# Kernel optimization log

Hardware: AMD Instinct MI355X
Metric: run time of the kernel (lower is better)

## Reference

```python
import jax, jax.numpy as jnp
import numpy as np

# Complete binary Huffman tree: V leaves, V-1 internal nodes, heap-indexed
# (node 0 = root, leaf i lives at heap index V-1+i, parent(n) = (n-1)//2).
V = 32768     # vocab size (leaves)
D = 15        # path depth = log2(V) internal nodes per leaf
DM = 1024     # input word-vector dim
B = 8         # batch of input word vectors
T = 1024      # target ids per batch item


def _build_paths():
    """paths[i, l] = heap index of the l-th internal node (leaf-to-root) on leaf i's path."""
    n = np.arange(V, dtype=np.int64) + (V - 1)  # leaf heap indices
    paths = np.zeros((V, D), dtype=np.int32)
    for lvl in range(D):
        n = (n - 1) // 2
        paths[:, lvl] = n
    return jnp.asarray(paths)


def setup_inputs() -> dict:
    key = jax.random.key(0)
    k1, k2, k3 = jax.random.split(key, 3)
    x = jax.random.normal(k1, (B, DM), dtype=jnp.float32)
    ids = jax.random.randint(k2, (B, T), 0, V)
    W = jax.random.normal(k3, (V - 1, DM), dtype=jnp.float32) * 0.02  # stacked Linear(DM,1) weights
    b = jnp.zeros((V - 1,), dtype=jnp.float32)                        # stacked Linear biases
    return {"x": x, "ids": ids, "paths": _build_paths(), "W": W, "b": b}


def reference(x, ids, paths, W, b):
    # node_idx: [B, T, D] internal-node heap indices along each target's path
    node_idx = paths[ids]
    Wp = W[node_idx]                 # [B, T, D, DM] gathered per-node weight rows
    bp = b[node_idx]                 # [B, T, D]
    # per-node Linear + bias: logit = w_node . x + b_node
    logits = jnp.einsum('btdk,bk->btd', Wp, x) + bp
    # product of sigmoid branch probabilities along the path -> [B, T]
    return jnp.prod(jax.nn.sigmoid(logits), axis=-1)
```

## Files before the change

kernel.cpp:

```cpp
#include <hip/hip_runtime.h>
#include <math.h>

#define V 32768
#define D 15
#define DM 1024
#define B 8
#define T 1024
#define NNODES (V - 1)
#define R 4

__global__ __launch_bounds__(256, 4) void hsm_logits_kernel(
    const float* __restrict__ x,
    const float* __restrict__ W,
    const float* __restrict__ bias,
    float* __restrict__ sig)
{
    __shared__ float4 xs[B * DM / 4];

    const float4* x4 = (const float4*)x;
    #pragma unroll
    for (int i = threadIdx.x; i < B * DM / 4; i += 256) xs[i] = x4[i];
    __syncthreads();

    const int wave = threadIdx.x >> 6;
    const int lane = threadIdx.x & 63;
    const int row0 = (blockIdx.x * 4 + wave) * R;

    const float4* Wb = (const float4*)W;
    const float4* Wr[R];
    #pragma unroll
    for (int r = 0; r < R; r++) {
        int row = row0 + r;
        if (row > NNODES - 1) row = NNODES - 1;
        Wr[r] = Wb + (size_t)row * 256;
    }

    float acc[R * B];
    #pragma unroll
    for (int i = 0; i < R * B; i++) acc[i] = 0.f;

    #pragma unroll
    for (int j = 0; j < 4; j++) {
        const int u = j * 64 + lane;
        float4 wv[R];
        #pragma unroll
        for (int r = 0; r < R; r++) wv[r] = Wr[r][u];
        float4 xv[B];
        #pragma unroll
        for (int b = 0; b < B; b++) xv[b] = xs[b * 256 + u];
        #pragma unroll
        for (int r = 0; r < R; r++) {
            #pragma unroll
            for (int b = 0; b < B; b++) {
                acc[r * 8 + b] += wv[r].x * xv[b].x + wv[r].y * xv[b].y +
                                  wv[r].z * xv[b].z + wv[r].w * xv[b].w;
            }
        }
    }

#define FOLD_LEVEL(MASK, NOUT)                                   \
    _Pragma("unroll")                                            \
    for (int i = 0; i < (NOUT); i++) {                           \
        const float lo = acc[2 * i];                             \
        const float hi = acc[2 * i + 1];                         \
        const float send = (lane & (MASK)) ? lo : hi;            \
        const float keep = (lane & (MASK)) ? hi : lo;            \
        acc[i] = keep + __shfl_xor(send, (MASK), 64);            \
    }
    FOLD_LEVEL(1, 16)
    FOLD_LEVEL(2, 8)
    FOLD_LEVEL(4, 4)
    FOLD_LEVEL(8, 2)
    FOLD_LEVEL(16, 1)
#undef FOLD_LEVEL
    acc[0] += __shfl_xor(acc[0], 32, 64);

    if (lane < 32) {
        const int r = lane >> 3;
        const int b = lane & 7;
        const int row = row0 + r;
        if (row < NNODES) {
            const float z = acc[0] + bias[row];
            sig[(size_t)row * B + b] = 1.f / (1.f + expf(-z));
        }
    }
}

__global__ __launch_bounds__(256) void hsm_prod_kernel(
    const int* __restrict__ ids,
    const int* __restrict__ paths,
    const float* __restrict__ sig,
    float* __restrict__ out)
{
    const int i = blockIdx.x * blockDim.x + threadIdx.x;
    if (i >= B * T) return;
    const int b = i / T;
    const int id = ids[i];
    const int* p = paths + (size_t)id * D;
    float prod = 1.f;
    #pragma unroll
    for (int d = 0; d < D; d++) {
        prod *= sig[(size_t)p[d] * B + b];
    }
    out[i] = prod;
}

extern "C" void kernel_launch(void* const* d_in, const int* in_sizes, int n_in,
                              void* d_out, int out_size, void* d_ws, size_t ws_size,
                              hipStream_t stream) {
    const float* x     = (const float*)d_in[0];
    const int*   ids   = (const int*)d_in[1];
    const int*   paths = (const int*)d_in[2];
    const float* W     = (const float*)d_in[3];
    const float* bias  = (const float*)d_in[4];
    float* out = (float*)d_out;
    float* sig = (float*)d_ws;

    const int rows_per_block = 4 * R;
    const int grid1 = (NNODES + rows_per_block - 1) / rows_per_block;
    hsm_logits_kernel<<<grid1, 256, 0, stream>>>(x, W, bias, sig);

    const int grid2 = (B * T + 255) / 256;
    hsm_prod_kernel<<<grid2, 256, 0, stream>>>(ids, paths, sig, out);
}
```

Measured before the change: 208.0 us.

## Software-pipeline W loads and process two row groups per wave

Each wave now handles 8 rows in two passes of 4. The W chunk for the next step, including the first chunk of the second pass, is prefetched into registers while the current chunk is being multiplied. The aim is to hide global-load latency and halve the grid, which also halves the number of times each block stages x into shared memory. The cost is higher register pressure from the double-buffered float4s, which could reduce occupancy.

```diff
diff --git a/kernel.cpp b/kernel.cpp
--- a/kernel.cpp
+++ b/kernel.cpp
@@ -22,41 +22,57 @@
     for (int i = threadIdx.x; i < B * DM / 4; i += 256) xs[i] = x4[i];
     __syncthreads();
 
-    const int wave = threadIdx.x >> 6;
+    const int wave = __builtin_amdgcn_readfirstlane(threadIdx.x >> 6);
     const int lane = threadIdx.x & 63;
-    const int row0 = (blockIdx.x * 4 + wave) * R;
+    const int rowbase = blockIdx.x * 32 + wave * 8;
 
     const float4* Wb = (const float4*)W;
-    const float4* Wr[R];
+
+    float4 wv[R], wvn[R];
+    float acc[R * B];
+
     #pragma unroll
     for (int r = 0; r < R; r++) {
-        int row = row0 + r;
+        int row = rowbase + r;
         if (row > NNODES - 1) row = NNODES - 1;
-        Wr[r] = Wb + (size_t)row * 256;
+        wv[r] = Wb[(size_t)row * 256 + lane];
     }
 
-    float acc[R * B];
-    #pragma unroll
-    for (int i = 0; i < R * B; i++) acc[i] = 0.f;
-
-    #pragma unroll
-    for (int j = 0; j < 4; j++) {
-        const int u = j * 64 + lane;
-        float4 wv[R];
+    auto run_pass = [&](int prow0, bool preload_next, int nrow0) {
         #pragma unroll
-        for (int r = 0; r < R; r++) wv[r] = Wr[r][u];
-        float4 xv[B];
+        for (int i = 0; i < R * B; i++) acc[i] = 0.f;
         #pragma unroll
-        for (int b = 0; b < B; b++) xv[b] = xs[b * 256 + u];
-        #pragma unroll
-        for (int r = 0; r < R; r++) {
+        for (int j = 0; j < 4; j++) {
+            if (j < 3) {
+                #pragma unroll
+                for (int r = 0; r < R; r++) {
+                    int row = prow0 + r;
+                    if (row > NNODES - 1) row = NNODES - 1;
+                    wvn[r] = Wb[(size_t)row * 256 + (j + 1) * 64 + lane];
+                }
+            } else if (preload_next) {
+                #pragma unroll
+                for (int r = 0; r < R; r++) {
+                    int row = nrow0 + r;
+                    if (row > NNODES - 1) row = NNODES - 1;
+                    wvn[r] = Wb[(size_t)row * 256 + lane];
+                }
+            }
+            float4 xv[B];
             #pragma unroll
-            for (int b = 0; b < B; b++) {
-                acc[r * 8 + b] += wv[r].x * xv[b].x + wv[r].y * xv[b].y +
-                                  wv[r].z * xv[b].z + wv[r].w * xv[b].w;
+            for (int b = 0; b < B; b++) xv[b] = xs[b * 256 + j * 64 + lane];
+            #pragma unroll
+            for (int r = 0; r < R; r++) {
+                #pragma unroll
+                for (int b = 0; b < B; b++) {
+                    acc[r * 8 + b] += wv[r].x * xv[b].x + wv[r].y * xv[b].y +
+                                      wv[r].z * xv[b].z + wv[r].w * xv[b].w;
+                }
             }
+            #pragma unroll
+            for (int r = 0; r < R; r++) wv[r] = wvn[r];
         }
-    }
+    };
 
 #define FOLD_LEVEL(MASK, NOUT)                                   \
     _Pragma("unroll")                                            \
@@ -67,23 +83,30 @@
         const float keep = (lane & (MASK)) ? hi : lo;            \
         acc[i] = keep + __shfl_xor(send, (MASK), 64);            \
     }
-    FOLD_LEVEL(1, 16)
-    FOLD_LEVEL(2, 8)
-    FOLD_LEVEL(4, 4)
-    FOLD_LEVEL(8, 2)
-    FOLD_LEVEL(16, 1)
+
+    auto fold_store = [&](int prow0) {
+        FOLD_LEVEL(1, 16)
+        FOLD_LEVEL(2, 8)
+        FOLD_LEVEL(4, 4)
+        FOLD_LEVEL(8, 2)
+        FOLD_LEVEL(16, 1)
+        acc[0] += __shfl_xor(acc[0], 32, 64);
+        if (lane < 32) {
+            const int r = lane >> 3;
+            const int b = lane & 7;
+            const int row = prow0 + r;
+            if (row < NNODES) {
+                const float z = acc[0] + bias[row];
+                sig[(size_t)row * B + b] = 1.f / (1.f + expf(-z));
+            }
+        }
+    };
+
+    run_pass(rowbase, true, rowbase + R);
+    fold_store(rowbase);
+    run_pass(rowbase + R, false, 0);
+    fold_store(rowbase + R);
 #undef FOLD_LEVEL
-    acc[0] += __shfl_xor(acc[0], 32, 64);
-
-    if (lane < 32) {
-        const int r = lane >> 3;
-        const int b = lane & 7;
-        const int row = row0 + r;
-        if (row < NNODES) {
-            const float z = acc[0] + bias[row];
-            sig[(size_t)row * B + b] = 1.f / (1.f + expf(-z));
-        }
-    }
 }
 
 __global__ __launch_bounds__(256) void hsm_prod_kernel(
@@ -116,8 +139,7 @@
     float* out = (float*)d_out;
     float* sig = (float*)d_ws;
 
-    const int rows_per_block = 4 * R;
-    const int grid1 = (NNODES + rows_per_block - 1) / rows_per_block;
+    const int grid1 = (V + 31) / 32;
     hsm_logits_kernel<<<grid1, 256, 0, stream>>>(x, W, bias, sig);
 
     const int grid2 = (B * T + 255) / 256;
```

Result: no change. 208.4 us (+0.2%).
